# Optimization experiments

Measured on AMD Instinct MI355X. Metric: run time of the kernel, lower is better.

## Reference

```python
import jax, jax.numpy as jnp
import numpy as np

B, S, V, E, H, F, L = 64, 32, 10000, 512, 512, 2048, 2
D = E + H  # concat(x, h) size; embedding_size == hidden_size so all layers share shapes


def setup_inputs() -> dict:
    key = jax.random.key(0)
    ks = jax.random.split(key, 10)

    def w(k, shape, fan):
        return jax.random.normal(k, shape, jnp.float32) / jnp.sqrt(jnp.float32(fan))

    tokens = jax.random.randint(ks[0], (B, S), 0, V)
    cnn_features = jax.random.normal(ks[1], (B, F), jnp.float32)
    emb = w(ks[2], (V, E), E)
    w_in = w(ks[3], (F, H), F)
    b_in = jnp.zeros((H,), jnp.float32)
    w_r = w(ks[4], (L, D, H), D)
    b_r = jnp.zeros((L, 1, H), jnp.float32)
    w_u = w(ks[5], (L, D, H), D)
    b_u = jnp.zeros((L, 1, H), jnp.float32)
    w_h = w(ks[6], (L, D, H), D)
    b_h = jnp.zeros((L, 1, H), jnp.float32)
    w_out = w(ks[7], (H, V), H)
    b_out = jnp.zeros((V,), jnp.float32)
    return dict(tokens=tokens, cnn_features=cnn_features, emb=emb, w_in=w_in, b_in=b_in,
                w_r=w_r, b_r=b_r, w_u=w_u, b_u=b_u, w_h=w_h, b_h=b_h,
                w_out=w_out, b_out=b_out)


def reference(tokens, cnn_features, emb, w_in, b_in, w_r, b_r, w_u, b_u, w_h, b_h, w_out, b_out):
    x = emb[tokens]                                   # [B, S, E]
    h0 = cnn_features @ w_in + b_in                   # [B, H] initial hidden state from CNN features
    seq = x
    for l in range(L):
        Wr, br = w_r[l], b_r[l]
        Wu, bu = w_u[l], b_u[l]
        Wh, bh = w_h[l], b_h[l]

        def step(h, xt):
            # xt: [B, D_in], h: [B, H] -- same GRU math as GRUCell.forward, batched
            xh = jnp.concatenate([xt, h], axis=-1)
            r = jax.nn.sigmoid(xh @ Wr + br)
            h_tilde = jnp.tanh(jnp.concatenate([xt, r * h], axis=-1) @ Wh + bh)
            u = jax.nn.sigmoid(xh @ Wu + bu)
            h_new = h * u + (1.0 - u) * h_tilde
            return h_new, h_new

        _, ys = jax.lax.scan(step, h0, jnp.swapaxes(seq, 0, 1))  # scan over time
        seq = jnp.swapaxes(ys, 0, 1)                  # [B, S, H]
    logits = seq @ w_out + b_out                      # [B, S, V]
    return logits
```

## Files before the change

### kernel.cpp

```cpp
#include <hip/hip_runtime.h>
#include <hip/hip_bf16.h>

typedef __hip_bfloat16 bf16;
typedef __attribute__((ext_vector_type(8))) short bf16x8s;
typedef __attribute__((ext_vector_type(4))) float f32x4;
typedef __attribute__((ext_vector_type(4))) int i32x4;

#define NB 64
#define NS 32
#define NV 10000
#define NE 512
#define NH 512
#define NF 2048
#define ND 1024

static __device__ __forceinline__ float bf2f(bf16 x) { return __bfloat162float(x); }
static __device__ __forceinline__ bf16 f2bf(float x) { return __float2bfloat16(x); }
static __device__ __forceinline__ short bfbits(float x) { bf16 h = f2bf(x); return *(short*)&h; }
static __device__ __forceinline__ f32x4 mfma16(bf16x8s a, bf16x8s b, f32x4 c) {
  return __builtin_amdgcn_mfma_f32_16x16x32_bf16(a, b, c, 0, 0, 0);
}

static __device__ __forceinline__ i32x4 ld16_sc(const void* p) {
  i32x4 r;
  asm volatile("global_load_dwordx4 %0, %1, off sc0 sc1" : "=v"(r) : "v"(p) : "memory");
  return r;
}
static __device__ __forceinline__ void st16_sc(void* p, i32x4 v) {
  asm volatile("global_store_dwordx4 %0, %1, off sc0 sc1" :: "v"(p), "v"(v) : "memory");
}
static __device__ __forceinline__ void stud_sc(void* p, unsigned v) {
  asm volatile("global_store_dword %0, %1, off sc0 sc1" :: "v"(p), "v"(v) : "memory");
}
static __device__ __forceinline__ void wait_vm0() {
  asm volatile("s_waitcnt vmcnt(0)" ::: "memory");
  __builtin_amdgcn_sched_barrier(0);
}
static __device__ __forceinline__ unsigned min4u(i32x4 a) {
  return min(min((unsigned)a[0], (unsigned)a[1]), min((unsigned)a[2], (unsigned)a[3]));
}

__device__ __forceinline__ f32x4 wave_tile16(const bf16* A, const bf16* BT,
                                             int lda, int K, int m0, int n0) {
  int lane = threadIdx.x & 63;
  int r = lane & 15, g = lane >> 4;
  const bf16* ap = A + (size_t)(m0 + r) * lda + g * 8;
  const bf16* bp = BT + (size_t)(n0 + r) * K + g * 8;
  f32x4 acc = {0.f, 0.f, 0.f, 0.f};
#pragma unroll 4
  for (int k = 0; k < K; k += 32) {
    bf16x8s a = *(const bf16x8s*)(ap + k);
    bf16x8s b = *(const bf16x8s*)(bp + k);
    acc = mfma16(a, b, acc);
  }
  return acc;
}

__global__ void k_cvt(const float* __restrict__ src, bf16* __restrict__ dst, int n) {
  int i = blockIdx.x * 256 + threadIdx.x;
  if (i < n) dst[i] = f2bf(src[i]);
}

__global__ void k_transpose(const float* __restrict__ src, bf16* __restrict__ dst,
                            int K, int N) {
  __shared__ float tile[32][33];
  int n0 = blockIdx.x * 32, k0 = blockIdx.y * 32;
  int tx = threadIdx.x & 31, ty = threadIdx.x >> 5;
  for (int i = ty; i < 32; i += 8) {
    int k = k0 + i, n = n0 + tx;
    tile[i][tx] = (k < K && n < N) ? src[(size_t)k * N + n] : 0.f;
  }
  __syncthreads();
  for (int i = ty; i < 32; i += 8) {
    int n = n0 + i, k = k0 + tx;
    if (n < N && k < K) dst[(size_t)n * K + k] = f2bf(tile[tx][i]);
  }
}

__global__ void k_transpose12(const float* __restrict__ w_r, const float* __restrict__ w_u,
                              const float* __restrict__ w_h, bf16* __restrict__ ruhT,
                              bf16* __restrict__ hhT, bf16* __restrict__ xT) {
  int z = blockIdx.z, l = z / 6, q = z % 6;
  const float* srcs[6] = {
    w_r + (size_t)l * ND * NH + (size_t)512 * NH,
    w_u + (size_t)l * ND * NH + (size_t)512 * NH,
    w_h + (size_t)l * ND * NH + (size_t)512 * NH,
    w_r + (size_t)l * ND * NH,
    w_u + (size_t)l * ND * NH,
    w_h + (size_t)l * ND * NH };
  bf16* dsts[6] = {
    ruhT + (size_t)l * 1024 * 512,
    ruhT + (size_t)l * 1024 * 512 + 512 * 512,
    hhT  + (size_t)l * 512 * 512,
    xT   + (size_t)l * 1536 * 512,
    xT   + (size_t)l * 1536 * 512 + 512 * 512,
    xT   + (size_t)l * 1536 * 512 + 1024 * 512 };
  const float* src = srcs[q];
  bf16* dst = dsts[q];
  __shared__ float tile[32][33];
  int n0 = blockIdx.x * 32, k0 = blockIdx.y * 32;
  int tx = threadIdx.x & 31, ty = threadIdx.x >> 5;
  for (int i = ty; i < 32; i += 8)
    tile[i][tx] = src[(size_t)(k0 + i) * NH + n0 + tx];
  __syncthreads();
  for (int i = ty; i < 32; i += 8)
    dst[(size_t)(n0 + i) * NH + k0 + tx] = f2bf(tile[tx][i]);
}

__global__ void k_bias3all(const float* __restrict__ br, const float* __restrict__ bu,
                           const float* __restrict__ bh, float* __restrict__ bias) {
  int i = blockIdx.x * 256 + threadIdx.x;
  if (i < 3072) {
    int l = i / 1536, c = i % 1536;
    const float* s = (c < 512) ? (br + l * 512 + c)
                   : (c < 1024 ? (bu + l * 512 + (c - 512)) : (bh + l * 512 + (c - 1024)));
    bias[i] = *s;
  }
}

__global__ void k_gemm_h0(const bf16* __restrict__ A, const bf16* __restrict__ BT,
                          const float* __restrict__ bias,
                          float* __restrict__ h0f, bf16* __restrict__ h0b) {
  int wid = blockIdx.x * 4 + (threadIdx.x >> 6);
  int mt = wid & 3, nt = wid >> 2;
  f32x4 acc = wave_tile16(A, BT, NF, NF, mt * 16, nt * 16);
  int lane = threadIdx.x & 63;
  int cl = lane & 15, g = lane >> 4;
  int col = nt * 16 + cl;
  float bv = bias[col];
#pragma unroll
  for (int j = 0; j < 4; j++) {
    int row = mt * 16 + g * 4 + j;
    float v = acc[j] + bv;
    h0f[(size_t)row * NH + col] = v;
    h0b[(size_t)row * NH + col] = f2bf(v);
  }
}

__global__ __launch_bounds__(512, 1)
void k_gru2(const bf16* __restrict__ w_ruh, const bf16* __restrict__ w_hh,
            const bf16* __restrict__ w_x, const float* __restrict__ bias3,
            const float* __restrict__ h0f, const bf16* __restrict__ h0b,
            const int* __restrict__ tokens, const float* __restrict__ emb,
            bf16* __restrict__ seq0, bf16* __restrict__ seq1,
            bf16* __restrict__ rh_all, float* __restrict__ pre,
            unsigned* __restrict__ flags, const float* __restrict__ w_out,
            const float* __restrict__ b_out, float* __restrict__ out) {
  __shared__ char lds[40960];
  const int tid = threadIdx.x;
  const int lane = tid & 63;
  const int wv = tid >> 6;
  const int cl = lane & 15, g4 = lane >> 4;
  const int bid = blockIdx.x;
  const int in0 = lane * 16;
  const int dsw = in0 ^ ((wv & 7) << 4);

  auto stage = [&](char* dst, const char* srcbase, int rstr) {
    i32x4 v0 = ld16_sc(srcbase + (size_t)wv * rstr + in0);
    i32x4 v1 = ld16_sc(srcbase + (size_t)(wv + 8) * rstr + in0);
    wait_vm0();
    *(i32x4*)(dst + wv * 1024 + dsw) = v0;
    *(i32x4*)(dst + (wv + 8) * 1024 + dsw) = v1;
  };
  auto afrag = [&](const char* panel, int kk) {
    return *(const bf16x8s*)(panel + cl * 1024 + ((kk * 64 + g4 * 16) ^ ((cl & 7) << 4)));
  };
  auto poll8 = [&](const unsigned* f, unsigned tgt) {
    if (tid == 0) {
      for (;;) {
        i32x4 a = ld16_sc(f);
        i32x4 b = ld16_sc(f + 4);
        wait_vm0();
        if (min(min4u(a), min4u(b)) >= tgt) break;
        __builtin_amdgcn_s_sleep(1);
      }
    }
    __syncthreads();
    __builtin_amdgcn_sched_barrier(0);
  };
  auto poll32 = [&](const unsigned* f, unsigned tgt) {
    if (tid == 0) {
      for (;;) {
        i32x4 a0 = ld16_sc(f),      a1 = ld16_sc(f + 4),  a2 = ld16_sc(f + 8),
              a3 = ld16_sc(f + 12), a4 = ld16_sc(f + 16), a5 = ld16_sc(f + 20),
              a6 = ld16_sc(f + 24), a7 = ld16_sc(f + 28);
        wait_vm0();
        unsigned mn = min(min(min(min4u(a0), min4u(a1)), min(min4u(a2), min4u(a3))),
                          min(min(min4u(a4), min4u(a5)), min(min4u(a6), min4u(a7))));
        if (mn >= tgt) break;
        __builtin_amdgcn_s_sleep(1);
      }
    }
    __syncthreads();
    __builtin_amdgcn_sched_barrier(0);
  };

  if (bid < 64) {
    const int l = bid >> 5, wg5 = bid & 31, mt = wg5 & 3, ng = wg5 >> 2;
    const bool is_u = (wv >= 4);
    const int wsub = wv & 3;
    const int c = (ng * 4 + wsub) * 16 + cl;
    const int colA = is_u ? 512 + c : c;
    char* hp = lds;
    char* rp = lds + 16384;
    float* ul = (float*)(lds + 32768);
    char* rout = lds + 36864;
    char* hout = lds + 38912;

    unsigned* f_h  = flags + (l * 4 + mt) * 32;
    unsigned* f_rh = flags + 256 + (l * 4 + mt) * 32;
    unsigned* f_pre = flags + 512 + (l * 4 + mt) * 32;

    bf16* seql = l ? seq1 : seq0;
    bf16* rh = rh_all + (size_t)l * 64 * 512;
    float* prel = pre + (size_t)l * 4 * 1536 * 64;

    bf16x8s bwA[16];
    { const bf16* pa = w_ruh + (size_t)l * 1024 * 512 + (size_t)colA * NH + g4 * 8;
#pragma unroll
      for (int k = 0; k < 16; k++) bwA[k] = *(const bf16x8s*)(pa + k * 32); }
    bf16x8s bwB[16];
    float h_reg[4];
    if (!is_u) {
      const bf16* pb = w_hh + (size_t)l * 512 * 512 + (size_t)c * NH + g4 * 8;
#pragma unroll
      for (int k = 0; k < 16; k++) bwB[k] = *(const bf16x8s*)(pb + k * 32);
#pragma unroll
      for (int j = 0; j < 4; j++)
        h_reg[j] = h0f[(size_t)(mt * 16 + g4 * 4 + j) * NH + c];
    }

    for (int t = 0; t < NS; t++) {
      if (tid == 0) {
        for (;;) {
          i32x4 p0 = ld16_sc(f_pre), p1 = ld16_sc(f_pre + 4), p2 = ld16_sc(f_pre + 8);
          i32x4 h0_, h1_;
          if (t) { h0_ = ld16_sc(f_h); h1_ = ld16_sc(f_h + 4); }
          wait_vm0();
          unsigned mnp = min(min(min4u(p0), min4u(p1)), min4u(p2));
          bool ok = mnp >= (unsigned)(t + 1);
          if (t) ok = ok && (min(min4u(h0_), min4u(h1_)) >= (unsigned)t);
          if (ok) break;
          __builtin_amdgcn_s_sleep(1);
        }
      }
      __syncthreads();
      __builtin_amdgcn_sched_barrier(0);
      const int slot = t & 3;
      i32x4 pv1 = ld16_sc(prel + ((size_t)(slot * 1536 + colA) * 64 + mt * 16 + g4 * 4));
      i32x4 pv2 = {0, 0, 0, 0};
      if (!is_u)
        pv2 = ld16_sc(prel + ((size_t)(slot * 1536 + 1024 + c) * 64 + mt * 16 + g4 * 4));
      if (t == 0) stage(hp, (const char*)(h0b + (size_t)mt * 16 * NH), 1024);
      else        stage(hp, (const char*)seql + ((size_t)(mt * 16) * NS + (t - 1)) * 1024,
                        NS * 1024);
      __syncthreads();
      f32x4 pA = *(f32x4*)&pv1;
      f32x4 pB = *(f32x4*)&pv2;
      {
        f32x4 acc = {0.f, 0.f, 0.f, 0.f};
#pragma unroll
        for (int kk = 0; kk < 16; kk++) acc = mfma16(afrag(hp, kk), bwA[kk], acc);
#pragma unroll
        for (int j = 0; j < 4; j++) {
          float gate = 1.f / (1.f + expf(-(acc[j] + pA[j])));
          if (is_u) {
            ul[(g4 * 4 + j) * 64 + wsub * 16 + cl] = gate;
          } else {
            bf16 o = f2bf(gate * h_reg[j]);
            *(unsigned short*)(rout + (g4 * 4 + j) * 128 + (wsub * 16 + cl) * 2)
              = *(unsigned short*)&o;
          }
        }
      }
      __syncthreads();
      {
        if (tid < 128) {
          int row = tid >> 3, ch = tid & 7;
          i32x4 v = *(i32x4*)(rout + row * 128 + ch * 16);
          st16_sc((char*)rh + (((size_t)(mt * 16 + row)) * NH + ng * 64 + ch * 8) * 2, v);
        }
        wait_vm0();
        __syncthreads();
        if (tid == 0) stud_sc(f_rh + ng, (unsigned)(t + 1));
      }
      poll8(f_rh, (unsigned)(t + 1));
      stage(rp, (const char*)(rh + (size_t)mt * 16 * NH), 1024);
      __syncthreads();
      if (!is_u) {
        f32x4 acc = {0.f, 0.f, 0.f, 0.f};
#pragma unroll
        for (int kk = 0; kk < 16; kk++) acc = mfma16(afrag(rp, kk), bwB[kk], acc);
#pragma unroll
        for (int j = 0; j < 4; j++) {
          float htil = tanhf(acc[j] + pB[j]);
          float u = ul[(g4 * 4 + j) * 64 + wsub * 16 + cl];
          float hnew = h_reg[j] * u + (1.f - u) * htil;
          h_reg[j] = hnew;
          bf16 hn = f2bf(hnew);
          *(unsigned short*)(hout + (g4 * 4 + j) * 128 + (wsub * 16 + cl) * 2)
            = *(unsigned short*)&hn;
        }
      }
      __syncthreads();
      {
        if (tid < 128) {
          int row = tid >> 3, ch = tid & 7;
          i32x4 v = *(i32x4*)(hout + row * 128 + ch * 16);
          st16_sc((char*)seql + (((size_t)(mt * 16 + row) * NS + t) * NH + ng * 64 + ch * 8) * 2, v);
        }
        wait_vm0();
        __syncthreads();
        if (tid == 0) {
          stud_sc(f_h + ng, (unsigned)(t + 1));
          if (l == 1) stud_sc(flags + 960 + mt * 8 + ng, (unsigned)(t + 1));
        }
      }
    }
  } else if (bid < 160) {
    const int wb = bid - 64;
    const int l = wb / 48, w48 = wb % 48, gg = w48 & 3, cw = w48 >> 2;
    char* xpan = lds;
    const int col = cw * 128 + wv * 16 + cl;
    float* prel = pre + (size_t)l * 4 * 1536 * 64;
    unsigned* f_h0g = flags + (0 * 4 + gg) * 32;
    unsigned* f_own = flags + (l * 4 + gg) * 32;
    unsigned* f_out = flags + 512 + (l * 4 + gg) * 32 + cw;

    bf16x8s wxw[16];
    { const bf16* pw = w_x + (size_t)l * 1536 * 512 + (size_t)col * 512 + g4 * 8;
#pragma unroll
      for (int kk = 0; kk < 16; kk++) wxw[kk] = *(const bf16x8s*)(pw + kk * 32); }
    const float bz = bias3[l * 1536 + col];

    for (int t = 0; t < NS; t++) {
      if (l == 1 || t >= 4) {
        if (tid == 0) {
          for (;;) {
            i32x4 a0 = {0,0,0,0}, a1 = {0,0,0,0}, b0 = {0,0,0,0}, b1 = {0,0,0,0};
            if (l == 1) { a0 = ld16_sc(f_h0g); a1 = ld16_sc(f_h0g + 4); }
            if (t >= 4) { b0 = ld16_sc(f_own); b1 = ld16_sc(f_own + 4); }
            wait_vm0();
            bool ok = true;
            if (l == 1) ok = min(min4u(a0), min4u(a1)) >= (unsigned)(t + 1);
            if (t >= 4) ok = ok && (min(min4u(b0), min4u(b1)) >= (unsigned)(t - 3));
            if (ok) break;
            __builtin_amdgcn_s_sleep(1);
          }
        }
        __syncthreads();
        __builtin_amdgcn_sched_barrier(0);
      }
      if (l == 0) {
#pragma unroll
        for (int rr = 0; rr < 2; rr++) {
          int r = wv + rr * 8;
          int tok = tokens[(gg * 16 + r) * NS + t];
          const float* ep = emb + (size_t)tok * NE + lane * 8;
          f32x4 v0 = *(const f32x4*)ep;
          f32x4 v1 = *(const f32x4*)(ep + 4);
          bf16x8s o;
#pragma unroll
          for (int j = 0; j < 4; j++) { o[j] = bfbits(v0[j]); o[4 + j] = bfbits(v1[j]); }
          *(i32x4*)(xpan + r * 1024 + dsw) = *(i32x4*)&o;
        }
      } else {
        stage(xpan, (const char*)seq0 + ((size_t)(gg * 16) * NS + t) * 1024, NS * 1024);
      }
      __syncthreads();
      f32x4 acc = {0.f, 0.f, 0.f, 0.f};
#pragma unroll
      for (int kk = 0; kk < 16; kk++) acc = mfma16(afrag(xpan, kk), wxw[kk], acc);
      {
        f32x4 o;
#pragma unroll
        for (int j = 0; j < 4; j++) o[j] = acc[j] + bz;
        st16_sc(prel + ((size_t)((t & 3) * 1536 + col) * 64 + gg * 16 + g4 * 4),
                *(i32x4*)&o);
      }
      wait_vm0();
      __syncthreads();
      if (tid == 0) stud_sc(f_out, (unsigned)(t + 1));
    }
  } else {
    const int oj = bid - 160;
    const int bh = oj & 1, cg = oj >> 1;
    char* aslab = lds;
    const int colb0 = (cg * 16 + wv * 2) * 16 + cl;
    const int colb1 = colb0 + 16;
    bf16x8s bw0[16], bw1[16];
#pragma unroll
    for (int kk = 0; kk < 16; kk++) {
      bf16x8s f0, f1;
#pragma unroll
      for (int jj = 0; jj < 8; jj++) {
        int k = kk * 32 + g4 * 8 + jj;
        f0[jj] = (colb0 < NV) ? bfbits(w_out[(size_t)k * NV + colb0]) : (short)0;
        f1[jj] = (colb1 < NV) ? bfbits(w_out[(size_t)k * NV + colb1]) : (short)0;
      }
      bw0[kk] = f0; bw1[kk] = f1;
    }
    const float bz0 = (colb0 < NV) ? b_out[colb0] : 0.f;
    const float bz1 = (colb1 < NV) ? b_out[colb1] : 0.f;
    unsigned* f1f = flags + 960;

    for (int t = 0; t < NS; t++) {
      poll32(f1f, (unsigned)(t + 1));
      {
        i32x4 vv[4];
        int rows[4], offs[4];
#pragma unroll
        for (int k4 = 0; k4 < 4; k4++) {
          int chunk = k4 * 512 + tid;
          rows[k4] = chunk >> 6;
          offs[k4] = (chunk & 63) * 16;
          vv[k4] = ld16_sc((const char*)seq1 +
                           ((size_t)(bh * 32 + rows[k4]) * NS + t) * 1024 + offs[k4]);
        }
        wait_vm0();
#pragma unroll
        for (int k4 = 0; k4 < 4; k4++)
          *(i32x4*)(aslab + rows[k4] * 1024 + (offs[k4] ^ ((rows[k4] & 7) << 4))) = vv[k4];
      }
      __syncthreads();
      f32x4 acc00 = {}, acc01 = {}, acc10 = {}, acc11 = {};
#pragma unroll
      for (int kk = 0; kk < 16; kk++) {
        int r0 = cl, r1 = 16 + cl;
        bf16x8s a0 = *(const bf16x8s*)(aslab + r0 * 1024 +
                                       ((kk * 64 + g4 * 16) ^ ((r0 & 7) << 4)));
        bf16x8s a1 = *(const bf16x8s*)(aslab + r1 * 1024 +
                                       ((kk * 64 + g4 * 16) ^ ((r1 & 7) << 4)));
        acc00 = mfma16(a0, bw0[kk], acc00);
        acc01 = mfma16(a0, bw1[kk], acc01);
        acc10 = mfma16(a1, bw0[kk], acc10);
        acc11 = mfma16(a1, bw1[kk], acc11);
      }
#pragma unroll
      for (int j = 0; j < 4; j++) {
        int b0r = bh * 32 + g4 * 4 + j;
        int b1r = b0r + 16;
        if (colb0 < NV) {
          out[((size_t)b0r * NS + t) * NV + colb0] = acc00[j] + bz0;
          out[((size_t)b1r * NS + t) * NV + colb0] = acc10[j] + bz0;
        }
        if (colb1 < NV) {
          out[((size_t)b0r * NS + t) * NV + colb1] = acc01[j] + bz1;
          out[((size_t)b1r * NS + t) * NV + colb1] = acc11[j] + bz1;
        }
      }
      __syncthreads();
    }
  }
}

extern "C" void kernel_launch(void* const* d_in, const int* in_sizes, int n_in,
                              void* d_out, int out_size, void* d_ws, size_t ws_size,
                              hipStream_t stream) {
  const int*   tokens = (const int*)d_in[0];
  const float* cnn    = (const float*)d_in[1];
  const float* emb    = (const float*)d_in[2];
  const float* w_in   = (const float*)d_in[3];
  const float* b_in   = (const float*)d_in[4];
  const float* w_r    = (const float*)d_in[5];
  const float* b_r    = (const float*)d_in[6];
  const float* w_u    = (const float*)d_in[7];
  const float* b_u    = (const float*)d_in[8];
  const float* w_h    = (const float*)d_in[9];
  const float* b_h    = (const float*)d_in[10];
  const float* w_out  = (const float*)d_in[11];
  const float* b_out  = (const float*)d_in[12];
  float* out = (float*)d_out;

  char* ws = (char*)d_ws;
  size_t off = 0;
  auto alloc = [&](size_t bytes) { char* p = ws + off; off += (bytes + 255) & ~(size_t)255; return p; };
  bf16*  seq0    = (bf16*) alloc((size_t)2048 * 512 * 2);
  bf16*  seq1    = (bf16*) alloc((size_t)2048 * 512 * 2);
  float* pre     = (float*)alloc((size_t)2 * 4 * 1536 * 64 * 4);
  float* h0f     = (float*)alloc((size_t)64 * 512 * 4);
  bf16*  h0b     = (bf16*) alloc((size_t)64 * 512 * 2);
  bf16*  rh_all  = (bf16*) alloc((size_t)2 * 64 * 512 * 2);
  float* bias3   = (float*)alloc((size_t)2 * 1536 * 4);
  bf16*  cnn_b   = (bf16*) alloc((size_t)64 * 2048 * 2);
  bf16*  w_in_T  = (bf16*) alloc((size_t)512 * 2048 * 2);
  bf16*  w_ruh_T = (bf16*) alloc((size_t)2 * 1024 * 512 * 2);
  bf16*  w_hh_T  = (bf16*) alloc((size_t)2 * 512 * 512 * 2);
  bf16*  w_x_T   = (bf16*) alloc((size_t)2 * 1536 * 512 * 2);
  unsigned* flags = (unsigned*)alloc(4096);
  (void)ws_size; (void)in_sizes; (void)n_in; (void)out_size;

  hipMemsetAsync(flags, 0, 4096, stream);

  k_cvt<<<512, 256, 0, stream>>>(cnn, cnn_b, 64 * 2048);
  k_transpose<<<dim3(16, 64), 256, 0, stream>>>(w_in, w_in_T, NF, NH);
  k_transpose12<<<dim3(16, 16, 12), 256, 0, stream>>>(w_r, w_u, w_h, w_ruh_T, w_hh_T, w_x_T);
  k_bias3all<<<12, 256, 0, stream>>>(b_r, b_u, b_h, bias3);

  k_gemm_h0<<<32, 256, 0, stream>>>(cnn_b, w_in_T, b_in, h0f, h0b);

  k_gru2<<<256, 512, 0, stream>>>(w_ruh_T, w_hh_T, w_x_T, bias3, h0f, h0b,
                                  tokens, emb, seq0, seq1, rh_all, pre, flags,
                                  w_out, b_out, out);
}
```

Measured before the change: 238.9 us.

## Fuse weight conversion and h0 GEMM into persistent GRU kernel

Removes the separate conversion, transpose, bias-gather and h0 GEMM launches. The GRU kernel now builds its register-resident bf16 weight fragments straight from the fp32 row-major weights with strided scalar loads. The layer-0 recurrent blocks compute h0 from the CNN features, splitting K across two wave groups and reducing through LDS, then signal the other blocks through a flag. This saves several launches and intermediate global buffers, at the cost of uncoalesced strided weight loads and h0 computation on the critical path before the recurrence.

```diff
diff --git a/kernel.cpp b/kernel.cpp
--- a/kernel.cpp
+++ b/kernel.cpp
@@ -26,11 +26,19 @@
   asm volatile("global_load_dwordx4 %0, %1, off sc0 sc1" : "=v"(r) : "v"(p) : "memory");
   return r;
 }
+static __device__ __forceinline__ float lddw_sc(const void* p) {
+  float r;
+  asm volatile("global_load_dword %0, %1, off sc0 sc1" : "=v"(r) : "v"(p) : "memory");
+  return r;
+}
 static __device__ __forceinline__ void st16_sc(void* p, i32x4 v) {
   asm volatile("global_store_dwordx4 %0, %1, off sc0 sc1" :: "v"(p), "v"(v) : "memory");
 }
 static __device__ __forceinline__ void stud_sc(void* p, unsigned v) {
   asm volatile("global_store_dword %0, %1, off sc0 sc1" :: "v"(p), "v"(v) : "memory");
+}
+static __device__ __forceinline__ void stus_sc(void* p, unsigned v) {
+  asm volatile("global_store_short %0, %1, off sc0 sc1" :: "v"(p), "v"(v) : "memory");
 }
 static __device__ __forceinline__ void wait_vm0() {
   asm volatile("s_waitcnt vmcnt(0)" ::: "memory");
@@ -40,108 +48,14 @@
   return min(min((unsigned)a[0], (unsigned)a[1]), min((unsigned)a[2], (unsigned)a[3]));
 }
 
-__device__ __forceinline__ f32x4 wave_tile16(const bf16* A, const bf16* BT,
-                                             int lda, int K, int m0, int n0) {
-  int lane = threadIdx.x & 63;
-  int r = lane & 15, g = lane >> 4;
-  const bf16* ap = A + (size_t)(m0 + r) * lda + g * 8;
-  const bf16* bp = BT + (size_t)(n0 + r) * K + g * 8;
-  f32x4 acc = {0.f, 0.f, 0.f, 0.f};
-#pragma unroll 4
-  for (int k = 0; k < K; k += 32) {
-    bf16x8s a = *(const bf16x8s*)(ap + k);
-    bf16x8s b = *(const bf16x8s*)(bp + k);
-    acc = mfma16(a, b, acc);
-  }
-  return acc;
-}
-
-__global__ void k_cvt(const float* __restrict__ src, bf16* __restrict__ dst, int n) {
-  int i = blockIdx.x * 256 + threadIdx.x;
-  if (i < n) dst[i] = f2bf(src[i]);
-}
-
-__global__ void k_transpose(const float* __restrict__ src, bf16* __restrict__ dst,
-                            int K, int N) {
-  __shared__ float tile[32][33];
-  int n0 = blockIdx.x * 32, k0 = blockIdx.y * 32;
-  int tx = threadIdx.x & 31, ty = threadIdx.x >> 5;
-  for (int i = ty; i < 32; i += 8) {
-    int k = k0 + i, n = n0 + tx;
-    tile[i][tx] = (k < K && n < N) ? src[(size_t)k * N + n] : 0.f;
-  }
-  __syncthreads();
-  for (int i = ty; i < 32; i += 8) {
-    int n = n0 + i, k = k0 + tx;
-    if (n < N && k < K) dst[(size_t)n * K + k] = f2bf(tile[tx][i]);
-  }
-}
-
-__global__ void k_transpose12(const float* __restrict__ w_r, const float* __restrict__ w_u,
-                              const float* __restrict__ w_h, bf16* __restrict__ ruhT,
-                              bf16* __restrict__ hhT, bf16* __restrict__ xT) {
-  int z = blockIdx.z, l = z / 6, q = z % 6;
-  const float* srcs[6] = {
-    w_r + (size_t)l * ND * NH + (size_t)512 * NH,
-    w_u + (size_t)l * ND * NH + (size_t)512 * NH,
-    w_h + (size_t)l * ND * NH + (size_t)512 * NH,
-    w_r + (size_t)l * ND * NH,
-    w_u + (size_t)l * ND * NH,
-    w_h + (size_t)l * ND * NH };
-  bf16* dsts[6] = {
-    ruhT + (size_t)l * 1024 * 512,
-    ruhT + (size_t)l * 1024 * 512 + 512 * 512,
-    hhT  + (size_t)l * 512 * 512,
-    xT   + (size_t)l * 1536 * 512,
-    xT   + (size_t)l * 1536 * 512 + 512 * 512,
-    xT   + (size_t)l * 1536 * 512 + 1024 * 512 };
-  const float* src = srcs[q];
-  bf16* dst = dsts[q];
-  __shared__ float tile[32][33];
-  int n0 = blockIdx.x * 32, k0 = blockIdx.y * 32;
-  int tx = threadIdx.x & 31, ty = threadIdx.x >> 5;
-  for (int i = ty; i < 32; i += 8)
-    tile[i][tx] = src[(size_t)(k0 + i) * NH + n0 + tx];
-  __syncthreads();
-  for (int i = ty; i < 32; i += 8)
-    dst[(size_t)(n0 + i) * NH + k0 + tx] = f2bf(tile[tx][i]);
-}
-
-__global__ void k_bias3all(const float* __restrict__ br, const float* __restrict__ bu,
-                           const float* __restrict__ bh, float* __restrict__ bias) {
-  int i = blockIdx.x * 256 + threadIdx.x;
-  if (i < 3072) {
-    int l = i / 1536, c = i % 1536;
-    const float* s = (c < 512) ? (br + l * 512 + c)
-                   : (c < 1024 ? (bu + l * 512 + (c - 512)) : (bh + l * 512 + (c - 1024)));
-    bias[i] = *s;
-  }
-}
-
-__global__ void k_gemm_h0(const bf16* __restrict__ A, const bf16* __restrict__ BT,
-                          const float* __restrict__ bias,
-                          float* __restrict__ h0f, bf16* __restrict__ h0b) {
-  int wid = blockIdx.x * 4 + (threadIdx.x >> 6);
-  int mt = wid & 3, nt = wid >> 2;
-  f32x4 acc = wave_tile16(A, BT, NF, NF, mt * 16, nt * 16);
-  int lane = threadIdx.x & 63;
-  int cl = lane & 15, g = lane >> 4;
-  int col = nt * 16 + cl;
-  float bv = bias[col];
-#pragma unroll
-  for (int j = 0; j < 4; j++) {
-    int row = mt * 16 + g * 4 + j;
-    float v = acc[j] + bv;
-    h0f[(size_t)row * NH + col] = v;
-    h0b[(size_t)row * NH + col] = f2bf(v);
-  }
-}
-
 __global__ __launch_bounds__(512, 1)
-void k_gru2(const bf16* __restrict__ w_ruh, const bf16* __restrict__ w_hh,
-            const bf16* __restrict__ w_x, const float* __restrict__ bias3,
-            const float* __restrict__ h0f, const bf16* __restrict__ h0b,
+void k_gru2(const float* __restrict__ w_r, const float* __restrict__ w_u,
+            const float* __restrict__ w_h, const float* __restrict__ b_r,
+            const float* __restrict__ b_u, const float* __restrict__ b_h,
+            const float* __restrict__ cnn, const float* __restrict__ w_in,
+            const float* __restrict__ b_in,
             const int* __restrict__ tokens, const float* __restrict__ emb,
+            float* __restrict__ h0f, bf16* __restrict__ h0b,
             bf16* __restrict__ seq0, bf16* __restrict__ seq1,
             bf16* __restrict__ rh_all, float* __restrict__ pre,
             unsigned* __restrict__ flags, const float* __restrict__ w_out,
@@ -194,13 +108,18 @@
     __syncthreads();
     __builtin_amdgcn_sched_barrier(0);
   };
+  auto bfrag = [&](const float* base, int k0, int col) {
+    bf16x8s o;
+#pragma unroll
+    for (int jj = 0; jj < 8; jj++) o[jj] = bfbits(base[(size_t)(k0 + jj) * 512 + col]);
+    return o;
+  };
 
   if (bid < 64) {
     const int l = bid >> 5, wg5 = bid & 31, mt = wg5 & 3, ng = wg5 >> 2;
     const bool is_u = (wv >= 4);
     const int wsub = wv & 3;
     const int c = (ng * 4 + wsub) * 16 + cl;
-    const int colA = is_u ? 512 + c : c;
     char* hp = lds;
     char* rp = lds + 16384;
     float* ul = (float*)(lds + 32768);
@@ -210,25 +129,71 @@
     unsigned* f_h  = flags + (l * 4 + mt) * 32;
     unsigned* f_rh = flags + 256 + (l * 4 + mt) * 32;
     unsigned* f_pre = flags + 512 + (l * 4 + mt) * 32;
+    unsigned* f_h0 = flags + 896 + mt * 8;
 
     bf16* seql = l ? seq1 : seq0;
     bf16* rh = rh_all + (size_t)l * 64 * 512;
     float* prel = pre + (size_t)l * 4 * 1536 * 64;
 
+    const float* wsrcA = (is_u ? w_u : w_r) + (size_t)l * ND * NH;
     bf16x8s bwA[16];
-    { const bf16* pa = w_ruh + (size_t)l * 1024 * 512 + (size_t)colA * NH + g4 * 8;
-#pragma unroll
-      for (int k = 0; k < 16; k++) bwA[k] = *(const bf16x8s*)(pa + k * 32); }
+#pragma unroll
+    for (int kk = 0; kk < 16; kk++)
+      bwA[kk] = bfrag(wsrcA, 512 + kk * 32 + g4 * 8, c);
     bf16x8s bwB[16];
+    if (!is_u) {
+      const float* wsrcB = w_h + (size_t)l * ND * NH;
+#pragma unroll
+      for (int kk = 0; kk < 16; kk++)
+        bwB[kk] = bfrag(wsrcB, 512 + kk * 32 + g4 * 8, c);
+    }
+
+    if (l == 0) {
+      const int ct = wv & 3, kh = wv >> 2;
+      const int col = ng * 64 + ct * 16 + cl;
+      f32x4 acc = {0.f, 0.f, 0.f, 0.f};
+      const float* arow = cnn + (size_t)(mt * 16 + cl) * NF + kh * 1024;
+#pragma unroll 4
+      for (int kk = 0; kk < 32; kk++) {
+        f32x4 a0 = *(const f32x4*)(arow + kk * 32 + g4 * 8);
+        f32x4 a1 = *(const f32x4*)(arow + kk * 32 + g4 * 8 + 4);
+        bf16x8s af;
+#pragma unroll
+        for (int j = 0; j < 4; j++) { af[j] = bfbits(a0[j]); af[4 + j] = bfbits(a1[j]); }
+        bf16x8s bf = bfrag(w_in, kh * 1024 + kk * 32 + g4 * 8, col);
+        acc = mfma16(af, bf, acc);
+      }
+      float* red = (float*)(lds + 32768);
+      if (kh == 1) {
+#pragma unroll
+        for (int j = 0; j < 4; j++) red[(ct * 64 + lane) * 4 + j] = acc[j];
+      }
+      __syncthreads();
+      if (kh == 0) {
+        float bz = b_in[col];
+#pragma unroll
+        for (int j = 0; j < 4; j++) {
+          float v = acc[j] + red[(ct * 64 + lane) * 4 + j] + bz;
+          int row = mt * 16 + g4 * 4 + j;
+          union { float f; unsigned u; } cv; cv.f = v;
+          stud_sc(h0f + (size_t)row * NH + col, cv.u);
+          bf16 hb_ = f2bf(v);
+          stus_sc(h0b + (size_t)row * NH + col, *(unsigned short*)&hb_);
+        }
+      }
+      wait_vm0();
+      __syncthreads();
+      if (tid == 0) stud_sc(f_h0 + ng, 1u);
+    }
+    poll8(f_h0, 1u);
     float h_reg[4];
     if (!is_u) {
-      const bf16* pb = w_hh + (size_t)l * 512 * 512 + (size_t)c * NH + g4 * 8;
-#pragma unroll
-      for (int k = 0; k < 16; k++) bwB[k] = *(const bf16x8s*)(pb + k * 32);
 #pragma unroll
       for (int j = 0; j < 4; j++)
-        h_reg[j] = h0f[(size_t)(mt * 16 + g4 * 4 + j) * NH + c];
-    }
+        h_reg[j] = lddw_sc(h0f + (size_t)(mt * 16 + g4 * 4 + j) * NH + c);
+      wait_vm0();
+    }
+    const int colA = is_u ? 512 + c : c;
 
     for (int t = 0; t < NS; t++) {
       if (tid == 0) {
@@ -327,11 +292,14 @@
     unsigned* f_own = flags + (l * 4 + gg) * 32;
     unsigned* f_out = flags + 512 + (l * 4 + gg) * 32 + cw;
 
+    const float* wsrc = (col < 512 ? w_r : (col < 1024 ? w_u : w_h)) + (size_t)l * ND * NH;
+    const int colw = col & 511;
     bf16x8s wxw[16];
-    { const bf16* pw = w_x + (size_t)l * 1536 * 512 + (size_t)col * 512 + g4 * 8;
-#pragma unroll
-      for (int kk = 0; kk < 16; kk++) wxw[kk] = *(const bf16x8s*)(pw + kk * 32); }
-    const float bz = bias3[l * 1536 + col];
+#pragma unroll
+    for (int kk = 0; kk < 16; kk++)
+      wxw[kk] = bfrag(wsrc, kk * 32 + g4 * 8, colw);
+    const float bz = (col < 512 ? b_r[l * 512 + colw]
+                     : (col < 1024 ? b_u[l * 512 + colw] : b_h[l * 512 + colw]));
 
     for (int t = 0; t < NS; t++) {
       if (l == 1 || t >= 4) {
@@ -481,25 +449,13 @@
   float* h0f     = (float*)alloc((size_t)64 * 512 * 4);
   bf16*  h0b     = (bf16*) alloc((size_t)64 * 512 * 2);
   bf16*  rh_all  = (bf16*) alloc((size_t)2 * 64 * 512 * 2);
-  float* bias3   = (float*)alloc((size_t)2 * 1536 * 4);
-  bf16*  cnn_b   = (bf16*) alloc((size_t)64 * 2048 * 2);
-  bf16*  w_in_T  = (bf16*) alloc((size_t)512 * 2048 * 2);
-  bf16*  w_ruh_T = (bf16*) alloc((size_t)2 * 1024 * 512 * 2);
-  bf16*  w_hh_T  = (bf16*) alloc((size_t)2 * 512 * 512 * 2);
-  bf16*  w_x_T   = (bf16*) alloc((size_t)2 * 1536 * 512 * 2);
   unsigned* flags = (unsigned*)alloc(4096);
   (void)ws_size; (void)in_sizes; (void)n_in; (void)out_size;
 
   hipMemsetAsync(flags, 0, 4096, stream);
 
-  k_cvt<<<512, 256, 0, stream>>>(cnn, cnn_b, 64 * 2048);
-  k_transpose<<<dim3(16, 64), 256, 0, stream>>>(w_in, w_in_T, NF, NH);
-  k_transpose12<<<dim3(16, 16, 12), 256, 0, stream>>>(w_r, w_u, w_h, w_ruh_T, w_hh_T, w_x_T);
-  k_bias3all<<<12, 256, 0, stream>>>(b_r, b_u, b_h, bias3);
-
-  k_gemm_h0<<<32, 256, 0, stream>>>(cnn_b, w_in_T, b_in, h0f, h0b);
-
-  k_gru2<<<256, 512, 0, stream>>>(w_ruh_T, w_hh_T, w_x_T, bias3, h0f, h0b,
-                                  tokens, emb, seq0, seq1, rh_all, pre, flags,
+  k_gru2<<<256, 512, 0, stream>>>(w_r, w_u, w_h, b_r, b_u, b_h,
+                                  cnn, w_in, b_in, tokens, emb,
+                                  h0f, h0b, seq0, seq1, rh_all, pre, flags,
                                   w_out, b_out, out);
 }
```

Result: slower. 256.3 us (+7.3%).
